# Optimization experiments

Measured on AMD Instinct MI355X. Metric: run time of the kernel, lower is better.

Reference implementation:

```python
import jax, jax.numpy as jnp
import numpy as np

B, DIM, H, W = 2, 192, 64, 64
HEADS = 4
EPS = 1e-12  # torch F.normalize eps


def conv2d(x, w, groups=1):
    # x: NCHW, w: OIHW, stride 1, SAME padding
    return jax.lax.conv_general_dilated(
        x, w, window_strides=(1, 1), padding='SAME',
        feature_group_count=groups,
        dimension_numbers=('NCHW', 'OIHW', 'NCHW'))


def setup_inputs() -> dict:
    key = jax.random.key(0)
    k1, k2, k3, k4 = jax.random.split(key, 4)
    x = jax.random.normal(k1, (B, DIM, H, W), dtype=jnp.float32)
    qkv_w = jax.random.normal(k2, (3 * DIM, DIM, 1, 1), dtype=jnp.float32) * 0.05
    dw_w = jax.random.normal(k3, (3 * DIM, 1, 3, 3), dtype=jnp.float32) * 0.05
    proj_w = jax.random.normal(k4, (DIM, DIM, 1, 1), dtype=jnp.float32) * 0.05
    temperature = jnp.ones((HEADS, 1, 1), dtype=jnp.float32)
    return {'x': x, 'qkv_w': qkv_w, 'dw_w': dw_w, 'proj_w': proj_w,
            'temperature': temperature}


def reference(x, qkv_w, dw_w, proj_w, temperature):
    b, dim, h, w = x.shape
    heads = temperature.shape[0]
    c = dim // heads  # per-head channels

    qkv = conv2d(conv2d(x, qkv_w), dw_w, groups=3 * dim)  # [b, 3*dim, h, w]
    q, k, v = jnp.split(qkv, 3, axis=1)

    def to_heads(t):
        # b (head c) h w -> b head (h w) c
        return t.reshape(b, heads, c, h * w).transpose(0, 1, 3, 2)

    q, k, v = to_heads(q), to_heads(k), to_heads(v)

    def l2norm(t):
        n = jnp.linalg.norm(t, axis=-1, keepdims=True)
        return t / jnp.maximum(n, EPS)

    q = l2norm(q)
    k = l2norm(k)

    # cosine attention with per-head learnable temperature
    attn = jnp.einsum('bnqc,bnkc->bnqk', q, k) * temperature[None]
    attn = jax.nn.softmax(attn, axis=-1)
    out = jnp.einsum('bnqk,bnkc->bnqc', attn, v)  # [b, head, hw, c]

    # b head (h w) c -> b (head c) h w
    out = out.transpose(0, 1, 3, 2).reshape(b, dim, h, w)
    return conv2d(out, proj_w)
```

## Files before the change

kernel.cpp:

```cpp
#include <hip/hip_runtime.h>
#include <cstdint>
#include <cstddef>

#define HW    4096
#define IMG   64
#define DIMC  192
#define NH    4
#define CH    48
#define CPAD  64
#define KVSPLIT 4
#define NTILE (HW / 64 / KVSPLIT)
#define LOG2E 1.4426950408889634f

typedef __bf16 bf16x8 __attribute__((ext_vector_type(8)));
typedef float  f32x4  __attribute__((ext_vector_type(4)));
typedef float  f32x16 __attribute__((ext_vector_type(16)));
typedef unsigned short u16x8 __attribute__((ext_vector_type(8)));
typedef unsigned int   u32x4 __attribute__((ext_vector_type(4)));

#if __has_builtin(__builtin_amdgcn_exp2f)
#define EXP2(x) __builtin_amdgcn_exp2f(x)
#else
#define EXP2(x) exp2f(x)
#endif

__device__ __forceinline__ unsigned short f2bf(float f) {
  unsigned int u = __builtin_bit_cast(unsigned int, f);
  u = (u + 0x7FFFu + ((u >> 16) & 1u)) >> 16;
  return (unsigned short)u;
}
__device__ __forceinline__ float bf2f(unsigned short u) {
  return __builtin_bit_cast(float, (unsigned int)u << 16);
}
__device__ __forceinline__ f32x4 mfma16(bf16x8 a, bf16x8 b, f32x4 c) {
  return __builtin_amdgcn_mfma_f32_16x16x32_bf16(a, b, c, 0, 0, 0);
}
__device__ __forceinline__ f32x16 mfma32(bf16x8 a, bf16x8 b, f32x16 c) {
  return __builtin_amdgcn_mfma_f32_32x32x16_bf16(a, b, c, 0, 0, 0);
}
__device__ __forceinline__ void gl16(const void* g, void* l) {
  __builtin_amdgcn_global_load_lds(
      (const __attribute__((address_space(1))) unsigned int*)g,
      (__attribute__((address_space(3))) unsigned int*)l, 16, 0, 0);
}
__device__ __forceinline__ unsigned int cvtpk(float lo, float hi) {
  unsigned int d;
  asm("v_cvt_pk_bf16_f32 %0, %1, %2" : "=v"(d) : "v"(lo), "v"(hi));
  return d;
}
__device__ __forceinline__ void swap32(unsigned int& a, unsigned int& b) {
  asm("v_permlane32_swap_b32 %0, %1" : "+v"(a), "+v"(b));
}

__global__ __launch_bounds__(256) void pack3_kernel(
    const float* __restrict__ x, const float* __restrict__ qkv_w,
    const float* __restrict__ proj_w, unsigned short* __restrict__ xb,
    unsigned short* __restrict__ wqkv, unsigned short* __restrict__ wproj) {
  const int bx = blockIdx.x, tid = threadIdx.x;
  if (bx < 128) {
    const int it = bx * 256 + tid;
    const int b = it >> 14;
    const int q4 = (it >> 12) & 3;
    const int p = it & 4095;
    const int c0 = q4 * 48;
    const float* src = x + ((size_t)b * DIMC + c0) * HW + p;
    float v[48];
    #pragma unroll
    for (int j = 0; j < 48; ++j) v[j] = src[(size_t)j * HW];
    #pragma unroll
    for (int g = 0; g < 6; ++g) {
      const int ch = c0 + g * 8;
      const int kc = ch >> 5, off = ch & 31;
      u16x8 gg;
      #pragma unroll
      for (int j = 0; j < 8; ++j) gg[j] = f2bf(v[g * 8 + j]);
      *(u16x8*)(xb + (((size_t)b * 6 + kc) * HW + p) * 32 + off) = gg;
    }
  } else {
    const int row = (bx - 128) * 256 + tid;
    if (row < 576) {
      const float* src = qkv_w + (size_t)row * DIMC;
      #pragma unroll
      for (int kc = 0; kc < 6; ++kc) {
        u16x8 g0, g1, g2, g3;
        #pragma unroll
        for (int j = 0; j < 8; ++j) {
          g0[j] = f2bf(src[kc * 32 + j]);      g1[j] = f2bf(src[kc * 32 + 8 + j]);
          g2[j] = f2bf(src[kc * 32 + 16 + j]); g3[j] = f2bf(src[kc * 32 + 24 + j]);
        }
        unsigned short* dst = wqkv + ((size_t)kc * 576 + row) * 32;
        *(u16x8*)dst = g0; *(u16x8*)(dst + 8) = g1;
        *(u16x8*)(dst + 16) = g2; *(u16x8*)(dst + 24) = g3;
      }
    } else {
      const int oc = row - 576;
      const float* src = proj_w + (size_t)oc * DIMC;
      #pragma unroll
      for (int kc = 0; kc < 6; ++kc) {
        u16x8 g0, g1, g2, g3;
        #pragma unroll
        for (int j = 0; j < 8; ++j) {
          g0[j] = f2bf(src[kc * 32 + j]);      g1[j] = f2bf(src[kc * 32 + 8 + j]);
          g2[j] = f2bf(src[kc * 32 + 16 + j]); g3[j] = f2bf(src[kc * 32 + 24 + j]);
        }
        unsigned short* dst = wproj + ((size_t)kc * DIMC + oc) * 32;
        *(u16x8*)dst = g0; *(u16x8*)(dst + 8) = g1;
        *(u16x8*)(dst + 16) = g2; *(u16x8*)(dst + 24) = g3;
      }
    }
  }
}

__global__ __launch_bounds__(256) void qkv_gemm_kernel(
    const unsigned short* __restrict__ xb, const unsigned short* __restrict__ wb,
    unsigned short* __restrict__ Cout) {
  const int tid = threadIdx.x;
  const int lane = tid & 63, wv = tid >> 6;
  const int l15 = lane & 15, l4 = lane >> 4;
  const int ocbase = blockIdx.x * 192;
  const int px0 = blockIdx.y * 64;
  const int b   = blockIdx.z;

  f32x4 acc[3][4];
  #pragma unroll
  for (int s = 0; s < 3; ++s)
    #pragma unroll
    for (int p = 0; p < 4; ++p) acc[s][p] = f32x4{0.f, 0.f, 0.f, 0.f};

  #pragma unroll
  for (int kc = 0; kc < 6; ++kc) {
    const unsigned short* xrow = xb + (((size_t)b * 6 + kc) * HW + px0 + l15) * 32 + l4 * 8;
    bf16x8 Bf[4];
    #pragma unroll
    for (int p = 0; p < 4; ++p) Bf[p] = *(const bf16x8*)(xrow + p * 512);
    #pragma unroll
    for (int s = 0; s < 3; ++s) {
      const int oc = ocbase + s * 64 + wv * 16 + l15;
      const bf16x8 af = *(const bf16x8*)(wb + ((size_t)kc * 576 + oc) * 32 + l4 * 8);
      #pragma unroll
      for (int p = 0; p < 4; ++p) acc[s][p] = mfma16(af, Bf[p], acc[s][p]);
    }
  }
  #pragma unroll
  for (int s = 0; s < 3; ++s) {
    unsigned short* Cb = Cout + ((size_t)b * 576 + ocbase + s * 64 + wv * 16) * HW + px0;
    #pragma unroll
    for (int p = 0; p < 4; ++p)
      #pragma unroll
      for (int r = 0; r < 4; ++r)
        Cb[(size_t)(l4 * 4 + r) * HW + p * 16 + l15] = f2bf(acc[s][p][r]);
  }
}

__global__ __launch_bounds__(256) void dw_conv3_kernel(
    const unsigned short* __restrict__ X, const float* __restrict__ W,
    unsigned short* __restrict__ Y) {
  __shared__ float T[66][72];
  const int bc = blockIdx.x;
  const int ch = bc % 576;
  const int tid = threadIdx.x;
  const unsigned short* Xb = X + (size_t)bc * HW;
  #pragma unroll
  for (int i = 0; i < 4; ++i) {
    const int idx = i * 256 + tid;
    const int row = idx >> 4, c4 = (idx & 15) << 2;
    const ushort4 u = *(const ushort4*)(Xb + row * 64 + c4);
    float4 f; f.x = bf2f(u.x); f.y = bf2f(u.y); f.z = bf2f(u.z); f.w = bf2f(u.w);
    *(float4*)&T[row + 1][c4 + 4] = f;
  }
  if (tid < 72) { T[0][tid] = 0.f; T[65][tid] = 0.f; }
  if (tid >= 128 && tid < 194) { const int r = tid - 128; T[r][3] = 0.f; T[r][68] = 0.f; }
  float w[9];
  #pragma unroll
  for (int i = 0; i < 9; ++i) w[i] = W[ch * 9 + i];
  __syncthreads();

  const int xx = tid & 63, ys = (tid >> 6) << 4;
  const int c = xx + 4;
  float a0 = T[ys][c - 1],     a1 = T[ys][c],     a2 = T[ys][c + 1];
  float b0 = T[ys + 1][c - 1], b1 = T[ys + 1][c], b2 = T[ys + 1][c + 1];
  unsigned short* Yb = Y + (size_t)bc * HW;
  #pragma unroll
  for (int k = 0; k < 16; ++k) {
    const float c0 = T[ys + k + 2][c - 1], c1 = T[ys + k + 2][c], c2 = T[ys + k + 2][c + 1];
    const float s = w[0] * a0 + w[1] * a1 + w[2] * a2
                  + w[3] * b0 + w[4] * b1 + w[5] * b2
                  + w[6] * c0 + w[7] * c1 + w[8] * c2;
    Yb[(ys + k) * 64 + xx] = f2bf(s);
    a0 = b0; a1 = b1; a2 = b2; b0 = c0; b1 = c1; b2 = c2;
  }
}

__global__ __launch_bounds__(256) void norm_pack3_kernel(
    const unsigned short* __restrict__ Dw, const float* __restrict__ temp,
    unsigned short* __restrict__ Qr, unsigned short* __restrict__ Kr,
    unsigned short* __restrict__ Vs) {
  const int px = blockIdx.x * 256 + threadIdx.x;
  const int sel = blockIdx.y >> 2, h = blockIdx.y & 3;
  const int b = blockIdx.z;
  const int bh = b * NH + h;
  const unsigned short* base = Dw + ((size_t)b * 576 + sel * DIMC + h * CH) * HW + px;

  float v[CH];
  if (sel == 2) {
    const int kt = px & ~63, kl = px & 63;
    #pragma unroll
    for (int c = 0; c < CH; ++c)
      Vs[((size_t)bh * CH + c) * HW + kt + (kl ^ ((c & 7) << 3))] = base[(size_t)c * HW];
    return;
  }
  float ss = 0.f;
  #pragma unroll
  for (int j = 0; j < CH; ++j) { v[j] = bf2f(base[(size_t)j * HW]); ss += v[j] * v[j]; }
  const u16x8 zz = {0, 0, 0, 0, 0, 0, 0, 0};
  if (sel == 0) {
    const float sc = temp[h] * LOG2E / fmaxf(sqrtf(ss), 1e-12f);
    u16x8 gr[8];
    #pragma unroll
    for (int g = 0; g < 6; ++g)
      #pragma unroll
      for (int j = 0; j < 8; ++j) gr[g][j] = f2bf(v[g * 8 + j] * sc);
    gr[6] = zz; gr[7] = zz;
    unsigned short* qrow = Qr + ((size_t)bh * HW + px) * CPAD;
    #pragma unroll
    for (int g = 0; g < 8; ++g) *(u16x8*)(qrow + g * 8) = gr[g];
  } else {
    const int ksw = (px & 3) | (((px >> 3) & 1) << 2);
    const float sc = 1.0f / fmaxf(sqrtf(ss), 1e-12f);
    u16x8 gr[8];
    #pragma unroll
    for (int g = 0; g < 6; ++g)
      #pragma unroll
      for (int j = 0; j < 8; ++j) gr[g][j] = f2bf(v[g * 8 + j] * sc);
    gr[6] = zz; gr[7] = zz;
    unsigned short* krow = Kr + ((size_t)bh * HW + px) * CPAD;
    #pragma unroll
    for (int g = 0; g < 8; ++g) *(u16x8*)(krow + (g ^ ksw) * 8) = gr[g];
  }
}

__global__ __launch_bounds__(256, 2) void flash8_kernel(
    const unsigned short* __restrict__ Qr,
    const unsigned short* __restrict__ Kr,
    const unsigned short* __restrict__ Vs,
    const float* __restrict__ temp,
    unsigned short* __restrict__ Opart, float* __restrict__ Lpart) {
  __shared__ __align__(16) union {
    struct { unsigned short Kl[2][4096]; unsigned short Vl[2][4096]; } s;
    float T[256][53];
  } lds;
  const int tid = threadIdx.x;
  const int lane = tid & 63, wv = tid >> 6;
  const int l31 = lane & 31, lhi = lane >> 5;
  const int bh = blockIdx.x, qt = blockIdx.y, sp = blockIdx.z;
  const int qb = qt * 256 + wv * 64;
  const float m = fabsf(temp[bh & 3]) * LOG2E * 1.05f + 0.1f;

  for (int i = tid; i < 1024; i += 256) {
    const unsigned short vv = (i < 64) ? (unsigned short)0x3F80 : (unsigned short)0;
    lds.s.Vl[0][3072 + i] = vv;
    lds.s.Vl[1][3072 + i] = vv;
  }

  const unsigned short* Qb = Qr + ((size_t)bh * HW + qb) * CPAD;
  bf16x8 qf[2][3];
  #pragma unroll
  for (int qb2 = 0; qb2 < 2; ++qb2)
    #pragma unroll
    for (int ci = 0; ci < 3; ++ci)
      qf[qb2][ci] = *(const bf16x8*)(Qb + (size_t)(qb2 * 32 + l31) * CPAD + ci * 16 + lhi * 8);

  const char* kg = (const char*)Kr + ((size_t)bh * HW + (size_t)sp * (HW / KVSPLIT)) * 128;
  const char* vg = (const char*)Vs + (size_t)bh * CH * HW * 2 + (size_t)sp * (HW / KVSPLIT) * 2;
  const int koA = tid * 16;
  const int vgA = (tid >> 3) * 8192 + (tid & 7) * 16;
  const int vgB = (32 + (tid >> 3)) * 8192 + (tid & 7) * 16;

  auto stage = [&](int buf, const char* kp, const char* vp) {
    char* kl = (char*)&lds.s.Kl[buf][0];
    gl16(kp + koA,        kl + koA);
    gl16(kp + 4096 + koA, kl + 4096 + koA);
    char* vl = (char*)&lds.s.Vl[buf][0];
    gl16(vp + vgA, vl + tid * 16);
    if (tid < 128) gl16(vp + vgB, vl + 4096 + tid * 16);
  };

  f32x16 o[2][2];
  #pragma unroll
  for (int cb = 0; cb < 2; ++cb)
    #pragma unroll
    for (int qb2 = 0; qb2 < 2; ++qb2)
      #pragma unroll
      for (int i = 0; i < 16; ++i) o[cb][qb2][i] = 0.f;
  f32x16 zin;
  #pragma unroll
  for (int i = 0; i < 16; ++i) zin[i] = -m;

  stage(0, kg, vg);
  kg += 8192; vg += 128;
  __syncthreads();
  int cur = 0;
  for (int t = 0; t < NTILE; ++t) {
    if (t + 1 < NTILE) { stage(cur ^ 1, kg, vg); kg += 8192; vg += 128; }
    const unsigned short* KL = &lds.s.Kl[cur][0];
    const unsigned short* VL = &lds.s.Vl[cur][0];

    f32x16 S[2][2];
    __builtin_amdgcn_s_setprio(1);
    #pragma unroll
    for (int kb = 0; kb < 2; ++kb) {
      const int krow = kb * 32 + l31;
      const int ksw = (krow & 3) | (((krow >> 3) & 1) << 2);
      bf16x8 kf[3];
      #pragma unroll
      for (int ci = 0; ci < 3; ++ci)
        kf[ci] = *(const bf16x8*)(KL + krow * 64 + (((ci * 2 + lhi) ^ ksw) * 8));
      #pragma unroll
      for (int qb2 = 0; qb2 < 2; ++qb2) {
        f32x16 acc = zin;
        #pragma unroll
        for (int ci = 0; ci < 3; ++ci) acc = mfma32(kf[ci], qf[qb2][ci], acc);
        S[kb][qb2] = acc;
      }
    }
    __builtin_amdgcn_s_setprio(0);

    #pragma unroll
    for (int kb = 0; kb < 2; ++kb) {
      #pragma unroll
      for (int qb2 = 0; qb2 < 2; ++qb2)
        #pragma unroll
        for (int i = 0; i < 16; ++i) S[kb][qb2][i] = EXP2(S[kb][qb2][i]);

      #pragma unroll
      for (int kh = 0; kh < 2; ++kh) {
        const int kc = kb * 2 + kh, rb = kh * 8;
        bf16x8 pb[2];
        #pragma unroll
        for (int qb2 = 0; qb2 < 2; ++qb2) {
          unsigned int w0 = cvtpk(S[kb][qb2][rb + 0], S[kb][qb2][rb + 1]);
          unsigned int w1 = cvtpk(S[kb][qb2][rb + 2], S[kb][qb2][rb + 3]);
          unsigned int w2 = cvtpk(S[kb][qb2][rb + 4], S[kb][qb2][rb + 5]);
          unsigned int w3 = cvtpk(S[kb][qb2][rb + 6], S[kb][qb2][rb + 7]);
          swap32(w0, w2);
          swap32(w1, w3);
          u32x4 ww = {w0, w1, w2, w3};
          pb[qb2] = __builtin_bit_cast(bf16x8, ww);
        }
        __builtin_amdgcn_s_setprio(1);
        #pragma unroll
        for (int cb = 0; cb < 2; ++cb) {
          const int crow = cb * 32 + l31;
          const bf16x8 vf = *(const bf16x8*)(VL + crow * 64 + (((kc * 2 + lhi) ^ (crow & 7)) * 8));
          #pragma unroll
          for (int qb2 = 0; qb2 < 2; ++qb2) o[cb][qb2] = mfma32(vf, pb[qb2], o[cb][qb2]);
        }
        __builtin_amdgcn_s_setprio(0);
      }
    }
    __syncthreads();
    cur ^= 1;
  }

  #pragma unroll
  for (int cb = 0; cb < 2; ++cb)
    #pragma unroll
    for (int qb2 = 0; qb2 < 2; ++qb2) {
      const int ql = wv * 64 + qb2 * 32 + l31;
      #pragma unroll
      for (int r = 0; r < 16; ++r) {
        const int c = cb * 32 + (r & 3) + 8 * (r >> 2) + 4 * lhi;
        if (c < 48) lds.T[ql][c] = o[cb][qb2][r];
      }
      if (lhi == 0) lds.T[ql][48] = o[1][qb2][8];
    }
  __syncthreads();
  {
    const int ql = tid;
    const int qg = qt * 256 + ql;
    float vv[48];
    #pragma unroll
    for (int c = 0; c < 48; ++c) vv[c] = lds.T[ql][c];
    const float Lv = lds.T[ql][48];
    unsigned short* Ob = Opart + ((size_t)(sp * 8 + bh) * HW + qg) * 48;
    #pragma unroll
    for (int g = 0; g < 6; ++g) {
      u16x8 gg;
      #pragma unroll
      for (int j = 0; j < 8; ++j) gg[j] = f2bf(vv[g * 8 + j]);
      *(u16x8*)(Ob + g * 8) = gg;
    }
    Lpart[(size_t)(sp * 8 + bh) * HW + qg] = Lv;
  }
}

__global__ __launch_bounds__(256) void proj_gemm_kernel(
    const unsigned short* __restrict__ Opart, const float* __restrict__ Lpart,
    const unsigned short* __restrict__ wb, float* __restrict__ Cout) {
  const int tid = threadIdx.x;
  const int lane = tid & 63, wv = tid >> 6;
  const int l15 = lane & 15, l4 = lane >> 4;
  const int px0 = blockIdx.y * 16;
  const int b   = blockIdx.z;

  bf16x8 Bf[6];
  #pragma unroll
  for (int kc = 0; kc < 6; ++kc) {
    const int ch0 = kc * 32 + l4 * 8;
    const int head = ch0 / 48, off = ch0 % 48;
    const int px = px0 + l15;
    float ls = 0.f;
    #pragma unroll
    for (int sp = 0; sp < 4; ++sp)
      ls += Lpart[(size_t)(sp * 8 + b * 4 + head) * HW + px];
    const float inv = 1.f / ls;
    float a8[8] = {};
    #pragma unroll
    for (int sp = 0; sp < 4; ++sp) {
      const u16x8 u = *(const u16x8*)(Opart +
          ((size_t)(sp * 8 + b * 4 + head) * HW + px) * 48 + off);
      #pragma unroll
      for (int j = 0; j < 8; ++j) a8[j] += bf2f(u[j]);
    }
    u16x8 g;
    #pragma unroll
    for (int j = 0; j < 8; ++j) g[j] = f2bf(a8[j] * inv);
    Bf[kc] = __builtin_bit_cast(bf16x8, g);
  }
  #pragma unroll
  for (int s = 0; s < 3; ++s) {
    const int oc = s * 64 + wv * 16 + l15;
    f32x4 acc = {0.f, 0.f, 0.f, 0.f};
    #pragma unroll
    for (int kc = 0; kc < 6; ++kc) {
      const bf16x8 af = *(const bf16x8*)(wb + ((size_t)kc * DIMC + oc) * 32 + l4 * 8);
      acc = mfma16(af, Bf[kc], acc);
    }
    float* Cb = Cout + ((size_t)b * DIMC + s * 64 + wv * 16) * HW + px0;
    #pragma unroll
    for (int r = 0; r < 4; ++r)
      Cb[(size_t)(l4 * 4 + r) * HW + l15] = acc[r];
  }
}

extern "C" void kernel_launch(void* const* d_in, const int* in_sizes, int n_in,
                              void* d_out, int out_size, void* d_ws, size_t ws_size,
                              hipStream_t stream) {
  const float* x      = (const float*)d_in[0];
  const float* qkv_w  = (const float*)d_in[1];
  const float* dw_w   = (const float*)d_in[2];
  const float* proj_w = (const float*)d_in[3];
  const float* temp   = (const float*)d_in[4];

  char* ws = (char*)d_ws;
  unsigned short* xb    = (unsigned short*)(ws);
  unsigned short* wqkv  = (unsigned short*)(ws + 3145728);
  unsigned short* wproj = (unsigned short*)(ws + 3366912);
  unsigned short* qkvb  = (unsigned short*)(ws + 3440640);
  unsigned short* dwb   = (unsigned short*)(ws + 12877824);
  unsigned short* Qr    = (unsigned short*)(ws + 22315008);
  unsigned short* Kr    = (unsigned short*)(ws + 26509312);
  unsigned short* Vs    = (unsigned short*)(ws + 30703616);
  unsigned short* Opart = (unsigned short*)(ws + 33849344);
  float*          Lpart = (float*)(ws + 46432256);

  pack3_kernel<<<dim3(131), 256, 0, stream>>>(x, qkv_w, proj_w, xb, wqkv, wproj);
  qkv_gemm_kernel<<<dim3(3, 64, 2), 256, 0, stream>>>(xb, wqkv, qkvb);
  dw_conv3_kernel<<<dim3(1152), 256, 0, stream>>>(qkvb, dw_w, dwb);
  norm_pack3_kernel<<<dim3(16, 12, 2), 256, 0, stream>>>(dwb, temp, Qr, Kr, Vs);
  flash8_kernel<<<dim3(8, 16, KVSPLIT), 256, 0, stream>>>(Qr, Kr, Vs, temp, Opart, Lpart);
  proj_gemm_kernel<<<dim3(1, 256, 2), 256, 0, stream>>>(Opart, Lpart, wproj, (float*)d_out);
}
```

Measured before the change: 79.13 us.

## Double KV split, raise flash occupancy, and shrink score register live range

Doubles the KV split of the attention kernel from 4 to 8, so there are twice as many blocks, each processing half as many key tiles. Launch bounds move to 3 blocks per SIMD, and the score computation is restructured so only one kb slice of S is live at a time, which cuts register pressure. The workspace is re-laid out so Opart aliases the dead xb/qkvb region, making room for the larger partial buffers. The projection kernel now reduces over twice as many partials, which adds read traffic and bf16 accumulation error.

```diff
diff --git a/kernel.cpp b/kernel.cpp
--- a/kernel.cpp
+++ b/kernel.cpp
@@ -8,7 +8,7 @@
 #define NH    4
 #define CH    48
 #define CPAD  64
-#define KVSPLIT 4
+#define KVSPLIT 8
 #define NTILE (HW / 64 / KVSPLIT)
 #define LOG2E 1.4426950408889634f
 
@@ -239,7 +239,7 @@
   }
 }
 
-__global__ __launch_bounds__(256, 2) void flash8_kernel(
+__global__ __launch_bounds__(256, 3) void flash9_kernel(
     const unsigned short* __restrict__ Qr,
     const unsigned short* __restrict__ Kr,
     const unsigned short* __restrict__ Vs,
@@ -292,9 +292,6 @@
     for (int qb2 = 0; qb2 < 2; ++qb2)
       #pragma unroll
       for (int i = 0; i < 16; ++i) o[cb][qb2][i] = 0.f;
-  f32x16 zin;
-  #pragma unroll
-  for (int i = 0; i < 16; ++i) zin[i] = -m;
 
   stage(0, kg, vg);
   kg += 8192; vg += 128;
@@ -305,8 +302,6 @@
     const unsigned short* KL = &lds.s.Kl[cur][0];
     const unsigned short* VL = &lds.s.Vl[cur][0];
 
-    f32x16 S[2][2];
-    __builtin_amdgcn_s_setprio(1);
     #pragma unroll
     for (int kb = 0; kb < 2; ++kb) {
       const int krow = kb * 32 + l31;
@@ -315,22 +310,23 @@
       #pragma unroll
       for (int ci = 0; ci < 3; ++ci)
         kf[ci] = *(const bf16x8*)(KL + krow * 64 + (((ci * 2 + lhi) ^ ksw) * 8));
+      f32x16 S[2];
+      __builtin_amdgcn_s_setprio(1);
       #pragma unroll
       for (int qb2 = 0; qb2 < 2; ++qb2) {
-        f32x16 acc = zin;
+        f32x16 acc;
+        #pragma unroll
+        for (int i = 0; i < 16; ++i) acc[i] = -m;
         #pragma unroll
         for (int ci = 0; ci < 3; ++ci) acc = mfma32(kf[ci], qf[qb2][ci], acc);
-        S[kb][qb2] = acc;
+        S[qb2] = acc;
       }
-    }
-    __builtin_amdgcn_s_setprio(0);
-
-    #pragma unroll
-    for (int kb = 0; kb < 2; ++kb) {
+      __builtin_amdgcn_s_setprio(0);
+
       #pragma unroll
       for (int qb2 = 0; qb2 < 2; ++qb2)
         #pragma unroll
-        for (int i = 0; i < 16; ++i) S[kb][qb2][i] = EXP2(S[kb][qb2][i]);
+        for (int i = 0; i < 16; ++i) S[qb2][i] = EXP2(S[qb2][i]);
 
       #pragma unroll
       for (int kh = 0; kh < 2; ++kh) {
@@ -338,10 +334,10 @@
         bf16x8 pb[2];
         #pragma unroll
         for (int qb2 = 0; qb2 < 2; ++qb2) {
-          unsigned int w0 = cvtpk(S[kb][qb2][rb + 0], S[kb][qb2][rb + 1]);
-          unsigned int w1 = cvtpk(S[kb][qb2][rb + 2], S[kb][qb2][rb + 3]);
-          unsigned int w2 = cvtpk(S[kb][qb2][rb + 4], S[kb][qb2][rb + 5]);
-          unsigned int w3 = cvtpk(S[kb][qb2][rb + 6], S[kb][qb2][rb + 7]);
+          unsigned int w0 = cvtpk(S[qb2][rb + 0], S[qb2][rb + 1]);
+          unsigned int w1 = cvtpk(S[qb2][rb + 2], S[qb2][rb + 3]);
+          unsigned int w2 = cvtpk(S[qb2][rb + 4], S[qb2][rb + 5]);
+          unsigned int w3 = cvtpk(S[qb2][rb + 6], S[qb2][rb + 7]);
           swap32(w0, w2);
           swap32(w1, w3);
           u32x4 ww = {w0, w1, w2, w3};
@@ -411,12 +407,12 @@
     const int px = px0 + l15;
     float ls = 0.f;
     #pragma unroll
-    for (int sp = 0; sp < 4; ++sp)
+    for (int sp = 0; sp < KVSPLIT; ++sp)
       ls += Lpart[(size_t)(sp * 8 + b * 4 + head) * HW + px];
     const float inv = 1.f / ls;
     float a8[8] = {};
     #pragma unroll
-    for (int sp = 0; sp < 4; ++sp) {
+    for (int sp = 0; sp < KVSPLIT; ++sp) {
       const u16x8 u = *(const u16x8*)(Opart +
           ((size_t)(sp * 8 + b * 4 + head) * HW + px) * 48 + off);
       #pragma unroll
@@ -453,21 +449,21 @@
   const float* temp   = (const float*)d_in[4];
 
   char* ws = (char*)d_ws;
-  unsigned short* xb    = (unsigned short*)(ws);
-  unsigned short* wqkv  = (unsigned short*)(ws + 3145728);
-  unsigned short* wproj = (unsigned short*)(ws + 3366912);
-  unsigned short* qkvb  = (unsigned short*)(ws + 3440640);
-  unsigned short* dwb   = (unsigned short*)(ws + 12877824);
-  unsigned short* Qr    = (unsigned short*)(ws + 22315008);
-  unsigned short* Kr    = (unsigned short*)(ws + 26509312);
-  unsigned short* Vs    = (unsigned short*)(ws + 30703616);
-  unsigned short* Opart = (unsigned short*)(ws + 33849344);
-  float*          Lpart = (float*)(ws + 46432256);
+  unsigned short* wqkv  = (unsigned short*)(ws);
+  unsigned short* wproj = (unsigned short*)(ws + 221184);
+  unsigned short* Qr    = (unsigned short*)(ws + 294912);
+  unsigned short* Kr    = (unsigned short*)(ws + 4489216);
+  unsigned short* Vs    = (unsigned short*)(ws + 8683520);
+  unsigned short* xb    = (unsigned short*)(ws + 11829248);
+  unsigned short* qkvb  = (unsigned short*)(ws + 14974976);
+  unsigned short* dwb   = (unsigned short*)(ws + 24412160);
+  unsigned short* Opart = (unsigned short*)(ws + 11829248);
+  float*          Lpart = (float*)(ws + 36995072);
 
   pack3_kernel<<<dim3(131), 256, 0, stream>>>(x, qkv_w, proj_w, xb, wqkv, wproj);
   qkv_gemm_kernel<<<dim3(3, 64, 2), 256, 0, stream>>>(xb, wqkv, qkvb);
   dw_conv3_kernel<<<dim3(1152), 256, 0, stream>>>(qkvb, dw_w, dwb);
   norm_pack3_kernel<<<dim3(16, 12, 2), 256, 0, stream>>>(dwb, temp, Qr, Kr, Vs);
-  flash8_kernel<<<dim3(8, 16, KVSPLIT), 256, 0, stream>>>(Qr, Kr, Vs, temp, Opart, Lpart);
+  flash9_kernel<<<dim3(8, 16, KVSPLIT), 256, 0, stream>>>(Qr, Kr, Vs, temp, Opart, Lpart);
   proj_gemm_kernel<<<dim3(1, 256, 2), 256, 0, stream>>>(Opart, Lpart, wproj, (float*)d_out);
 }
```

Result: slower. 90.93 us (+14.9%).
